# Optimization experiments

Hardware: AMD Instinct MI355X
Metric: run time of the kernel (lower is better)

The kernel has to match this reference:

```python
import jax, jax.numpy as jnp
import numpy as np

N = 256
FEAT = 1024           # box_head.fc7.out_features
HID_REL = 256         # RelationProposalNetwork hidden_dim
GCN_HID = 256         # gcn_hidden
HEADS = 4
NUM_PARTS = 20
OUT = NUM_PARTS + 1
TOPK = 3
IN_GCN = FEAT + 4


def setup_inputs() -> dict:
    key = jax.random.key(0)
    ks = jax.random.split(key, 16)
    features = jax.random.normal(ks[0], (N, FEAT), jnp.float32)
    # valid pixel-space boxes (x1, y1, x2, y2) inside an 800x800 image
    xy = jax.random.uniform(ks[1], (N, 2), jnp.float32, 0.0, 700.0)
    wh = jax.random.uniform(ks[2], (N, 2), jnp.float32, 8.0, 100.0)
    boxes = jnp.concatenate([xy, xy + wh], axis=1)
    s = 0.02
    W_fc1 = jax.random.normal(ks[3], (2 * FEAT + 4, HID_REL), jnp.float32) * s
    b_fc1 = jnp.zeros((HID_REL,), jnp.float32)
    W_fc2 = jax.random.normal(ks[4], (HID_REL, 1), jnp.float32) * s
    b_fc2 = jnp.zeros((1,), jnp.float32)
    W1 = jax.random.normal(ks[5], (IN_GCN, HEADS * GCN_HID), jnp.float32) * s
    a_src1 = jax.random.normal(ks[6], (HEADS, GCN_HID), jnp.float32) * s
    a_dst1 = jax.random.normal(ks[7], (HEADS, GCN_HID), jnp.float32) * s
    b1 = jnp.zeros((HEADS * GCN_HID,), jnp.float32)
    W2 = jax.random.normal(ks[8], (HEADS * GCN_HID, OUT), jnp.float32) * s
    a_src2 = jax.random.normal(ks[9], (1, OUT), jnp.float32) * s
    a_dst2 = jax.random.normal(ks[10], (1, OUT), jnp.float32) * s
    b2 = jnp.zeros((OUT,), jnp.float32)
    return {
        "features": features, "boxes": boxes,
        "W_fc1": W_fc1, "b_fc1": b_fc1, "W_fc2": W_fc2, "b_fc2": b_fc2,
        "W1": W1, "a_src1": a_src1, "a_dst1": a_dst1, "b1": b1,
        "W2": W2, "a_src2": a_src2, "a_dst2": a_dst2, "b2": b2,
        "img_h": 800, "img_w": 800,
    }


def _gat_layer(x, W, a_src, a_dst, bias, s, t, n, heads, ch):
    # PyG GATConv: message flows edge_index[0] (s) -> edge_index[1] (t),
    # softmax over incoming edges of each target node t.
    h = (x @ W).reshape(n, heads, ch)                       # [n, H, C]
    e = jax.nn.leaky_relu(
        jnp.einsum("ehc,hc->eh", h[s], a_src)
        + jnp.einsum("ehc,hc->eh", h[t], a_dst), 0.2)        # [E, H]
    m = jnp.full((n, heads), -1e30, e.dtype).at[t].max(e)    # segment max
    p = jnp.exp(e - m[t])
    denom = jax.ops.segment_sum(p, t, num_segments=n)
    alpha = p / denom[t]                                     # [E, H]
    out = jax.ops.segment_sum(alpha[:, :, None] * h[s], t, num_segments=n)
    return out.reshape(n, heads * ch) + bias


def _forward(features, boxes, W_fc1, b_fc1, W_fc2, b_fc2,
             W1, a_src1, a_dst1, b1, W2, a_src2, a_dst2, b2, img_h, img_w):
    n = features.shape[0]
    # --- RelationProposalNetwork: dense O(N^2) pairwise MLP ---
    f1 = jnp.broadcast_to(features[:, None, :], (n, n, FEAT))
    f2 = jnp.broadcast_to(features[None, :, :], (n, n, FEAT))
    geom = jnp.abs(boxes[:, None, :] - boxes[None, :, :])    # [n, n, 4]
    pair = jnp.concatenate([f1, f2, geom], axis=-1)          # [n, n, 2052]
    hid = jax.nn.relu(pair @ W_fc1 + b_fc1)                  # [n, n, 256]
    rel = (hid @ W_fc2 + b_fc2)[..., 0]                      # [n, n]
    # --- top-k graph construction (drop first = self, as in source) ---
    idx = jax.lax.top_k(rel, TOPK + 1)[1][:, 1:]             # [n, topk]
    s_e = jnp.repeat(jnp.arange(n), TOPK)                    # edge_index[0]
    t_e = idx.reshape(-1)                                    # edge_index[1]
    loops = jnp.arange(n)                                    # GATConv add_self_loops
    s_e = jnp.concatenate([s_e, loops])
    t_e = jnp.concatenate([t_e, loops])
    # --- normalized box geometry node features ---
    scale = jnp.array([img_w, img_h, img_w, img_h], jnp.float32)
    nb = boxes / scale
    geomn = jnp.stack([nb[:, 0], nb[:, 1], nb[:, 2] - nb[:, 0], nb[:, 3] - nb[:, 1]], axis=1)
    gcn_in = jnp.concatenate([features, geomn], axis=1)      # [n, 1028]
    # --- AttentionalGCN: GAT(heads=4) -> ReLU -> GAT(heads=1) ---
    h1 = jax.nn.relu(_gat_layer(gcn_in, W1, a_src1, a_dst1, b1, s_e, t_e, n, HEADS, GCN_HID))
    logits = _gat_layer(h1, W2, a_src2, a_dst2, b2, s_e, t_e, n, 1, OUT)
    return logits


def reference(features, boxes, W_fc1, b_fc1, W_fc2, b_fc2,
              W1, a_src1, a_dst1, b1, W2, a_src2, a_dst2, b2, img_h, img_w):
    logits = _forward(features, boxes, W_fc1, b_fc1, W_fc2, b_fc2,
                      W1, a_src1, a_dst1, b1, W2, a_src2, a_dst2, b2, img_h, img_w)
    labels = jnp.argmax(logits, axis=1)
    return logits, labels
```

## Files before the change

kernel.cpp:

```cpp
#include <hip/hip_runtime.h>
#include <math.h>

#define NN 256
#define FEAT 1024
#define HIDR 256
#define HEADS 4
#define GCNH 256
#define M1 1024
#define OUTC 21
#define MAXDEG (NN + 1)
#define KC 16
#define KCH (FEAT / KC)
#define RB 16
#define FCOLS 1536

__global__ __launch_bounds__(256) void k_big(
        const float* __restrict__ feat, const float* __restrict__ Wfc1,
        const float* __restrict__ W1, float* __restrict__ P) {
    __shared__ float fS[RB][KCH];
    int rg = blockIdx.x, cgy = blockIdx.y, kc = blockIdx.z;
    int tid = threadIdx.x;
    int r0 = rg * RB, k0 = kc * KCH;
    for (int x = tid; x < RB * KCH; x += 256) {
        int r = x >> 6, kk = x & (KCH - 1);
        fS[r][kk] = feat[(size_t)(r0 + r) * FEAT + k0 + kk];
    }
    __syncthreads();
    int gc = cgy * 512 + tid * 2;
    const float* pW;
    int ld;
    if (gc < 256)      { pW = Wfc1 + (size_t)k0 * HIDR + gc;                  ld = HIDR; }
    else if (gc < 512) { pW = Wfc1 + (size_t)(FEAT + k0) * HIDR + (gc - 256); ld = HIDR; }
    else               { pW = W1   + (size_t)k0 * M1 + (gc - 512);            ld = M1;   }
    float2 acc[RB];
#pragma unroll
    for (int r = 0; r < RB; r++) { acc[r].x = 0.f; acc[r].y = 0.f; }
    float2 w0 = *(const float2*)(pW);
    float2 w1 = *(const float2*)(pW + ld);
    float2 w2 = *(const float2*)(pW + 2 * ld);
    float2 w3 = *(const float2*)(pW + 3 * ld);
    for (int kk = 0; kk < KCH; kk += 4) {
        pW += 4 * ld;
        float2 n0 = *(const float2*)(pW);
        float2 n1 = *(const float2*)(pW + ld);
        float2 n2 = *(const float2*)(pW + 2 * ld);
        float2 n3 = *(const float2*)(pW + 3 * ld);
#pragma unroll
        for (int r = 0; r < RB; r++) {
            float4 f = *(const float4*)&fS[r][kk];
            acc[r].x = fmaf(f.x, w0.x, acc[r].x); acc[r].y = fmaf(f.x, w0.y, acc[r].y);
            acc[r].x = fmaf(f.y, w1.x, acc[r].x); acc[r].y = fmaf(f.y, w1.y, acc[r].y);
            acc[r].x = fmaf(f.z, w2.x, acc[r].x); acc[r].y = fmaf(f.z, w2.y, acc[r].y);
            acc[r].x = fmaf(f.w, w3.x, acc[r].x); acc[r].y = fmaf(f.w, w3.y, acc[r].y);
        }
        w0 = n0; w1 = n1; w2 = n2; w3 = n3;
    }
    float* Pp = P + ((size_t)kc * NN + r0) * FCOLS + gc;
#pragma unroll
    for (int r = 0; r < RB; r++)
        *(float2*)(Pp + (size_t)r * FCOLS) = acc[r];
}

__global__ __launch_bounds__(384) void k_redfix(
        const float* __restrict__ P, const float* __restrict__ bfc1,
        const float* __restrict__ boxes, const int* __restrict__ imh,
        const int* __restrict__ imw, const float* __restrict__ W1,
        const float* __restrict__ as1, const float* __restrict__ ad1,
        float* __restrict__ A, float* __restrict__ BT4,
        float* __restrict__ hpre, float* __restrict__ es1,
        float* __restrict__ ed1, float* __restrict__ geomn) {
    __shared__ float gS[4];
    int row = blockIdx.x, tid = threadIdx.x;
    int c4 = tid * 4;
    const float* p = P + (size_t)row * FCOLS + c4;
    const size_t str = (size_t)NN * FCOLS;
    float4 a0 = *(const float4*)(p);
    float4 a1 = *(const float4*)(p + str);
    float4 a2 = *(const float4*)(p + 2 * str);
    float4 a3 = *(const float4*)(p + 3 * str);
#pragma unroll
    for (int q = 4; q < KC; q += 4) {
        float4 t0 = *(const float4*)(p + (size_t)q * str);
        float4 t1 = *(const float4*)(p + (size_t)(q + 1) * str);
        float4 t2 = *(const float4*)(p + (size_t)(q + 2) * str);
        float4 t3 = *(const float4*)(p + (size_t)(q + 3) * str);
        a0.x += t0.x; a0.y += t0.y; a0.z += t0.z; a0.w += t0.w;
        a1.x += t1.x; a1.y += t1.y; a1.z += t1.z; a1.w += t1.w;
        a2.x += t2.x; a2.y += t2.y; a2.z += t2.z; a2.w += t2.w;
        a3.x += t3.x; a3.y += t3.y; a3.z += t3.z; a3.w += t3.w;
    }
    float4 s;
    s.x = (a0.x + a1.x) + (a2.x + a3.x);
    s.y = (a0.y + a1.y) + (a2.y + a3.y);
    s.z = (a0.z + a1.z) + (a2.z + a3.z);
    s.w = (a0.w + a1.w) + (a2.w + a3.w);
    if (tid == 0) {
        float w = (float)imw[0], h = (float)imh[0];
        float x1 = boxes[row * 4 + 0] / w, y1 = boxes[row * 4 + 1] / h;
        float x2 = boxes[row * 4 + 2] / w, y2 = boxes[row * 4 + 3] / h;
        gS[0] = x1; gS[1] = y1; gS[2] = x2 - x1; gS[3] = y2 - y1;
        geomn[row * 4 + 0] = x1;
        geomn[row * 4 + 1] = y1;
        geomn[row * 4 + 2] = x2 - x1;
        geomn[row * 4 + 3] = y2 - y1;
    }
    __syncthreads();
    if (c4 < 256) {
        float4 b = *(const float4*)(bfc1 + c4);
        s.x += b.x; s.y += b.y; s.z += b.z; s.w += b.w;
        *(float4*)(A + (size_t)row * HIDR + c4) = s;
    } else if (c4 < 512) {
        int kk = c4 - 256;
        *(float4*)(BT4 + (size_t)(kk >> 2) * (NN * 4) + row * 4) = s;
    } else {
        int ch = c4 - 512;
        float g0 = gS[0], g1 = gS[1], g2 = gS[2], g3 = gS[3];
        float4 wv;
        wv = *(const float4*)(W1 + (size_t)(FEAT + 0) * M1 + ch);
        s.x = fmaf(g0, wv.x, s.x); s.y = fmaf(g0, wv.y, s.y);
        s.z = fmaf(g0, wv.z, s.z); s.w = fmaf(g0, wv.w, s.w);
        wv = *(const float4*)(W1 + (size_t)(FEAT + 1) * M1 + ch);
        s.x = fmaf(g1, wv.x, s.x); s.y = fmaf(g1, wv.y, s.y);
        s.z = fmaf(g1, wv.z, s.z); s.w = fmaf(g1, wv.w, s.w);
        wv = *(const float4*)(W1 + (size_t)(FEAT + 2) * M1 + ch);
        s.x = fmaf(g2, wv.x, s.x); s.y = fmaf(g2, wv.y, s.y);
        s.z = fmaf(g2, wv.z, s.z); s.w = fmaf(g2, wv.w, s.w);
        wv = *(const float4*)(W1 + (size_t)(FEAT + 3) * M1 + ch);
        s.x = fmaf(g3, wv.x, s.x); s.y = fmaf(g3, wv.y, s.y);
        s.z = fmaf(g3, wv.z, s.z); s.w = fmaf(g3, wv.w, s.w);
        *(float4*)(hpre + (size_t)row * M1 + ch) = s;
        float4 a = *(const float4*)(as1 + ch);
        float4 b = *(const float4*)(ad1 + ch);
        float ps = s.x * a.x + s.y * a.y + s.z * a.z + s.w * a.w;
        float pd = s.x * b.x + s.y * b.y + s.z * b.z + s.w * b.w;
#pragma unroll
        for (int o = 32; o > 0; o >>= 1) {
            ps += __shfl_down(ps, o);
            pd += __shfl_down(pd, o);
        }
        if ((tid & 63) == 0) {
            int head = (tid - 128) >> 6;
            es1[row * 4 + head] = ps;
            ed1[row * 4 + head] = pd;
        }
    }
}

__global__ __launch_bounds__(512) void k_reltopk(
        const float* __restrict__ A, const float* __restrict__ BT4,
        const float* __restrict__ boxes, const float* __restrict__ Wfc1,
        const float* __restrict__ Wfc2, int* __restrict__ idxTop) {
    __shared__ float As[HIDR], w2s[HIDR], wg0[HIDR], wg1[HIDR], wg2[HIDR], wg3[HIDR];
    __shared__ float sval[512];
    __shared__ unsigned long long swk[8];
    __shared__ int win;
    int i = blockIdx.x, tid = threadIdx.x;
    int j = tid & 255, half = tid >> 8;
    if (tid < 256) {
        As[tid]  = A[i * HIDR + tid];
        w2s[tid] = Wfc2[tid];
        wg0[tid] = Wfc1[(size_t)(2 * FEAT + 0) * HIDR + tid];
    } else {
        int q = tid - 256;
        wg1[q] = Wfc1[(size_t)(2 * FEAT + 1) * HIDR + q];
        wg2[q] = Wfc1[(size_t)(2 * FEAT + 2) * HIDR + q];
        wg3[q] = Wfc1[(size_t)(2 * FEAT + 3) * HIDR + q];
    }
    float bi0 = boxes[i * 4 + 0], bi1 = boxes[i * 4 + 1];
    float bi2 = boxes[i * 4 + 2], bi3 = boxes[i * 4 + 3];
    float g0 = fabsf(bi0 - boxes[j * 4 + 0]);
    float g1 = fabsf(bi1 - boxes[j * 4 + 1]);
    float g2 = fabsf(bi2 - boxes[j * 4 + 2]);
    float g3 = fabsf(bi3 - boxes[j * 4 + 3]);
    __syncthreads();
    int k0 = half * 128;
    const float* pB = BT4 + (size_t)(k0 >> 2) * (NN * 4) + j * 4;
    float acc = 0.f;
    for (int kk = k0; kk < k0 + 128; kk += 4) {
        float4 a4 = *(const float4*)&As[kk];
        float4 w4 = *(const float4*)&w2s[kk];
        float4 q0 = *(const float4*)&wg0[kk];
        float4 q1 = *(const float4*)&wg1[kk];
        float4 q2 = *(const float4*)&wg2[kk];
        float4 q3 = *(const float4*)&wg3[kk];
        float4 b4 = *(const float4*)pB;
        pB += NN * 4;
        float v;
        v = a4.x + b4.x; v = fmaf(g0, q0.x, v); v = fmaf(g1, q1.x, v);
        v = fmaf(g2, q2.x, v); v = fmaf(g3, q3.x, v);
        acc = fmaf(fmaxf(v, 0.f), w4.x, acc);
        v = a4.y + b4.y; v = fmaf(g0, q0.y, v); v = fmaf(g1, q1.y, v);
        v = fmaf(g2, q2.y, v); v = fmaf(g3, q3.y, v);
        acc = fmaf(fmaxf(v, 0.f), w4.y, acc);
        v = a4.z + b4.z; v = fmaf(g0, q0.z, v); v = fmaf(g1, q1.z, v);
        v = fmaf(g2, q2.z, v); v = fmaf(g3, q3.z, v);
        acc = fmaf(fmaxf(v, 0.f), w4.z, acc);
        v = a4.w + b4.w; v = fmaf(g0, q0.w, v); v = fmaf(g1, q1.w, v);
        v = fmaf(g2, q2.w, v); v = fmaf(g3, q3.w, v);
        acc = fmaf(fmaxf(v, 0.f), w4.w, acc);
    }
    sval[tid] = acc;
    __syncthreads();
    if (tid < 256) sval[tid] = sval[tid] + sval[tid + 256];
    __syncthreads();
    for (int r = 0; r < 4; r++) {
        unsigned long long key = 0ULL;
        if (tid < 256) {
            unsigned u = __float_as_uint(sval[tid]);
            u = (u & 0x80000000u) ? ~u : (u | 0x80000000u);
            key = ((unsigned long long)u << 32) | (unsigned)(NN - 1 - tid);
        }
#pragma unroll
        for (int o = 32; o > 0; o >>= 1) {
            unsigned long long nk = __shfl_down(key, o);
            if (nk > key) key = nk;
        }
        if ((tid & 63) == 0) swk[tid >> 6] = key;
        __syncthreads();
        if (tid == 0) {
            unsigned long long m = swk[0];
#pragma unroll
            for (int q = 1; q < 8; q++) if (swk[q] > m) m = swk[q];
            int wj = NN - 1 - (int)(m & 0xFFFFFFFFu);
            win = wj;
            if (r > 0) idxTop[i * 3 + (r - 1)] = wj;
        }
        __syncthreads();
        if (tid == win) sval[tid] = -1e38f;
        __syncthreads();
    }
}

__global__ __launch_bounds__(256) void k_gat1h2(
        const float* __restrict__ idxTopF, const float* __restrict__ hpre,
        const float* __restrict__ es1, const float* __restrict__ ed1,
        const float* __restrict__ b1, const float* __restrict__ W2,
        const float* __restrict__ as2, const float* __restrict__ ad2,
        int* __restrict__ deg, int* __restrict__ inlist,
        float* __restrict__ h2, float* __restrict__ es2,
        float* __restrict__ ed2) {
    const int* idxTop = (const int*)idxTopF;
    __shared__ int pfx[NN];
    __shared__ int lst[MAXDEG];
    __shared__ int dgS;
    __shared__ float sc[MAXDEG * 4];
    __shared__ float mh[4], dh[4];
    __shared__ float sh[M1];
    __shared__ float part[12 * OUTC];
    __shared__ float h2row[OUTC];
    int t = blockIdx.x, tid = threadIdx.x;
    int f = (idxTop[tid * 3 + 0] == t) | (idxTop[tid * 3 + 1] == t)
          | (idxTop[tid * 3 + 2] == t);
    pfx[tid] = f;
    __syncthreads();
    for (int o = 1; o < NN; o <<= 1) {
        int add = (tid >= o) ? pfx[tid - o] : 0;
        __syncthreads();
        pfx[tid] += add;
        __syncthreads();
    }
    if (f) {
        lst[pfx[tid] - 1] = tid;
        inlist[t * MAXDEG + (pfx[tid] - 1)] = tid;
    }
    if (tid == NN - 1) {
        int d = pfx[NN - 1];
        lst[d] = t;
        inlist[t * MAXDEG + d] = t;
        dgS = d + 1;
        deg[t] = d + 1;
    }
    __syncthreads();
    int dg = dgS;
    for (int p = tid; p < dg * 4; p += 256) {
        int e = p >> 2, h = p & 3;
        int s = lst[e];
        float v = es1[s * 4 + h] + ed1[t * 4 + h];
        sc[p] = v >= 0.f ? v : 0.2f * v;
    }
    __syncthreads();
    if (tid < 4) {
        float m = -1e30f;
        for (int e = 0; e < dg; e++) m = fmaxf(m, sc[e * 4 + tid]);
        float s = 0.f;
        for (int e = 0; e < dg; e++) s += expf(sc[e * 4 + tid] - m);
        mh[tid] = m; dh[tid] = s;
    }
    __syncthreads();
    for (int p = tid; p < dg * 4; p += 256) {
        int h = p & 3;
        sc[p] = expf(sc[p] - mh[h]) / dh[h];
    }
    __syncthreads();
    float acc[4] = {0.f, 0.f, 0.f, 0.f};
    for (int e = 0; e < dg; e++) {
        int s = lst[e];
        const float* hs = hpre + (size_t)s * M1;
#pragma unroll
        for (int q = 0; q < 4; q++)
            acc[q] = fmaf(sc[e * 4 + q], hs[q * GCNH + tid], acc[q]);
    }
#pragma unroll
    for (int q = 0; q < 4; q++) {
        int c = q * GCNH + tid;
        sh[c] = fmaxf(acc[q] + b1[c], 0.f);
    }
    __syncthreads();
    if (tid < 252) {
        int o = tid % OUTC, p = tid / OUTC;
        float a2 = 0.f;
        for (int d = p; d < M1; d += 12)
            a2 = fmaf(sh[d], W2[d * OUTC + o], a2);
        part[p * OUTC + o] = a2;
    }
    __syncthreads();
    if (tid < OUTC) {
        float s = 0.f;
        for (int p = 0; p < 12; p++) s += part[p * OUTC + tid];
        h2[t * OUTC + tid] = s;
        h2row[tid] = s;
    }
    __syncthreads();
    if (tid == 0) {
        float s = 0.f, dd = 0.f;
        for (int k = 0; k < OUTC; k++) {
            s = fmaf(h2row[k], as2[k], s);
            dd = fmaf(h2row[k], ad2[k], dd);
        }
        es2[t] = s; ed2[t] = dd;
    }
}

__global__ __launch_bounds__(64) void k_gat2(
        const float* __restrict__ h2, const float* __restrict__ es2,
        const float* __restrict__ ed2, const int* __restrict__ deg,
        const int* __restrict__ inlist, const float* __restrict__ b2,
        float* __restrict__ out) {
    __shared__ float sc[MAXDEG];
    __shared__ float md[2];
    __shared__ float lv[OUTC];
    int t = blockIdx.x, tid = threadIdx.x;
    int dg = deg[t];
    float edt = ed2[t];
    for (int p = tid; p < dg; p += 64) {
        int s = inlist[t * MAXDEG + p];
        float v = es2[s] + edt;
        sc[p] = v >= 0.f ? v : 0.2f * v;
    }
    __syncthreads();
    if (tid == 0) {
        float m = -1e30f;
        for (int e = 0; e < dg; e++) m = fmaxf(m, sc[e]);
        float s = 0.f;
        for (int e = 0; e < dg; e++) s += expf(sc[e] - m);
        md[0] = m; md[1] = s;
    }
    __syncthreads();
    if (tid < OUTC) {
        float acc = 0.f;
        for (int e = 0; e < dg; e++) {
            int s = inlist[t * MAXDEG + e];
            float a = expf(sc[e] - md[0]) / md[1];
            acc = fmaf(a, h2[s * OUTC + tid], acc);
        }
        float v = acc + b2[tid];
        out[t * OUTC + tid] = v;
        lv[tid] = v;
    }
    __syncthreads();
    if (tid == 0) {
        int best = 0;
        float bv = lv[0];
        for (int o = 1; o < OUTC; o++)
            if (lv[o] > bv) { bv = lv[o]; best = o; }
        out[NN * OUTC + t] = (float)best;
    }
}

extern "C" void kernel_launch(void* const* d_in, const int* in_sizes, int n_in,
                              void* d_out, int out_size, void* d_ws,
                              size_t ws_size, hipStream_t stream) {
    const float* feat  = (const float*)d_in[0];
    const float* boxes = (const float*)d_in[1];
    const float* Wfc1  = (const float*)d_in[2];
    const float* bfc1  = (const float*)d_in[3];
    const float* Wfc2  = (const float*)d_in[4];
    const float* bfc2  = (const float*)d_in[5];   (void)bfc2;
    const float* W1    = (const float*)d_in[6];
    const float* as1   = (const float*)d_in[7];
    const float* ad1   = (const float*)d_in[8];
    const float* b1    = (const float*)d_in[9];
    const float* W2    = (const float*)d_in[10];
    const float* as2   = (const float*)d_in[11];
    const float* ad2   = (const float*)d_in[12];
    const float* b2    = (const float*)d_in[13];
    const int*   imh   = (const int*)d_in[14];
    const int*   imw   = (const int*)d_in[15];

    float* ws = (float*)d_ws;
    float* P     = ws;  ws += KC * NN * FCOLS;
    float* A     = ws;  ws += NN * HIDR;
    float* BT4   = ws;  ws += NN * HIDR;
    float* hpre  = ws;  ws += NN * M1;
    float* es1   = ws;  ws += NN * 4;
    float* ed1   = ws;  ws += NN * 4;
    float* h2    = ws;  ws += NN * OUTC;
    float* es2   = ws;  ws += NN;
    float* ed2   = ws;  ws += NN;
    float* geomn = ws;  ws += NN * 4;
    int* deg     = (int*)ws;
    int* inlist  = deg + NN;
    int* idxTop  = inlist + NN * MAXDEG;

    float* out = (float*)d_out;

    k_big<<<dim3(NN / RB, 3, KC), 256, 0, stream>>>(feat, Wfc1, W1, P);
    k_redfix<<<NN, 384, 0, stream>>>(P, bfc1, boxes, imh, imw, W1, as1, ad1,
                                     A, BT4, hpre, es1, ed1, geomn);
    k_reltopk<<<NN, 512, 0, stream>>>(A, BT4, boxes, Wfc1, Wfc2, idxTop);
    k_gat1h2<<<NN, 256, 0, stream>>>((const float*)idxTop, hpre, es1, ed1,
                                     b1, W2, as2, ad2, deg, inlist,
                                     h2, es2, ed2);
    k_gat2<<<NN, 64, 0, stream>>>(h2, es2, ed2, deg, inlist, b2, out);
}
```

Baseline: 164.8 us.

## Fuse four post-GEMM kernels into one persistent kernel with grid barriers

Merges the reduce/fixup, relation top-k, first GAT layer and second GAT layer kernels into one 256-block kernel that uses an atomic-counter grid barrier between stages. The barrier counter is reset inside the preceding GEMM kernel. Per-node in-edge lists stay in shared memory instead of going through global deg/inlist arrays, and the A vector is kept in LDS. This removes three kernel launch gaps and some global traffic. In exchange it relies on all 256 blocks being co-resident and adds spin-wait cost at each barrier.

Result: slower. 193.1 us (+17.2%).

```diff
diff --git a/kernel.cpp b/kernel.cpp
--- a/kernel.cpp
+++ b/kernel.cpp
@@ -16,7 +16,11 @@
 
 __global__ __launch_bounds__(256) void k_big(
         const float* __restrict__ feat, const float* __restrict__ Wfc1,
-        const float* __restrict__ W1, float* __restrict__ P) {
+        const float* __restrict__ W1, float* __restrict__ P,
+        unsigned* bar) {
+    if (blockIdx.x == 0 && blockIdx.y == 0 && blockIdx.z == 0 &&
+        threadIdx.x == 0)
+        *bar = 0u;
     __shared__ float fS[RB][KCH];
     int rg = blockIdx.x, cgy = blockIdx.y, kc = blockIdx.z;
     int tid = threadIdx.x;
@@ -61,103 +65,130 @@
         *(float2*)(Pp + (size_t)r * FCOLS) = acc[r];
 }
 
-__global__ __launch_bounds__(384) void k_redfix(
+__device__ __forceinline__ void gsync(unsigned* bar, unsigned expected) {
+    __syncthreads();
+    if (threadIdx.x == 0) {
+        __threadfence();
+        atomicAdd(bar, 1u);
+        while (atomicAdd(bar, 0u) < expected)
+            __builtin_amdgcn_s_sleep(2);
+        __threadfence();
+    }
+    __syncthreads();
+}
+
+__global__ __launch_bounds__(512, 4) void k_fused(
         const float* __restrict__ P, const float* __restrict__ bfc1,
         const float* __restrict__ boxes, const int* __restrict__ imh,
         const int* __restrict__ imw, const float* __restrict__ W1,
         const float* __restrict__ as1, const float* __restrict__ ad1,
-        float* __restrict__ A, float* __restrict__ BT4,
-        float* __restrict__ hpre, float* __restrict__ es1,
-        float* __restrict__ ed1, float* __restrict__ geomn) {
+        const float* __restrict__ Wfc1, const float* __restrict__ Wfc2,
+        const float* __restrict__ b1, const float* __restrict__ W2,
+        const float* __restrict__ as2, const float* __restrict__ ad2,
+        const float* __restrict__ b2,
+        float* __restrict__ BT4, float* __restrict__ hpre,
+        float* __restrict__ es1, float* __restrict__ ed1,
+        int* __restrict__ idxTop, float* __restrict__ h2,
+        float* __restrict__ es2, float* __restrict__ ed2,
+        unsigned* bar, float* __restrict__ out) {
     __shared__ float gS[4];
+    __shared__ float As[HIDR], w2s[HIDR];
+    __shared__ float wg0[HIDR], wg1[HIDR], wg2[HIDR], wg3[HIDR];
+    __shared__ float sval[512];
+    __shared__ unsigned long long swk[8];
+    __shared__ int win;
+    __shared__ int pfx[NN];
+    __shared__ int lst[MAXDEG];
+    __shared__ int dgS;
+    __shared__ float sc[MAXDEG * 4];
+    __shared__ float mh[4], dh[4];
+    __shared__ float sh[M1];
+    __shared__ float part[24 * OUTC];
+    __shared__ float h2row[OUTC];
+    __shared__ float scD[MAXDEG];
+    __shared__ float md[2];
+    __shared__ float lv[OUTC];
+
     int row = blockIdx.x, tid = threadIdx.x;
+
     int c4 = tid * 4;
-    const float* p = P + (size_t)row * FCOLS + c4;
-    const size_t str = (size_t)NN * FCOLS;
-    float4 a0 = *(const float4*)(p);
-    float4 a1 = *(const float4*)(p + str);
-    float4 a2 = *(const float4*)(p + 2 * str);
-    float4 a3 = *(const float4*)(p + 3 * str);
-#pragma unroll
-    for (int q = 4; q < KC; q += 4) {
-        float4 t0 = *(const float4*)(p + (size_t)q * str);
-        float4 t1 = *(const float4*)(p + (size_t)(q + 1) * str);
-        float4 t2 = *(const float4*)(p + (size_t)(q + 2) * str);
-        float4 t3 = *(const float4*)(p + (size_t)(q + 3) * str);
-        a0.x += t0.x; a0.y += t0.y; a0.z += t0.z; a0.w += t0.w;
-        a1.x += t1.x; a1.y += t1.y; a1.z += t1.z; a1.w += t1.w;
-        a2.x += t2.x; a2.y += t2.y; a2.z += t2.z; a2.w += t2.w;
-        a3.x += t3.x; a3.y += t3.y; a3.z += t3.z; a3.w += t3.w;
-    }
-    float4 s;
-    s.x = (a0.x + a1.x) + (a2.x + a3.x);
-    s.y = (a0.y + a1.y) + (a2.y + a3.y);
-    s.z = (a0.z + a1.z) + (a2.z + a3.z);
-    s.w = (a0.w + a1.w) + (a2.w + a3.w);
+    bool actA = (tid < 384);
+    float4 s4;
+    if (actA) {
+        const float* p = P + (size_t)row * FCOLS + c4;
+        const size_t str = (size_t)NN * FCOLS;
+        float4 a0 = *(const float4*)(p);
+        float4 a1 = *(const float4*)(p + str);
+        float4 a2 = *(const float4*)(p + 2 * str);
+        float4 a3 = *(const float4*)(p + 3 * str);
+#pragma unroll
+        for (int q = 4; q < KC; q += 4) {
+            float4 t0 = *(const float4*)(p + (size_t)q * str);
+            float4 t1 = *(const float4*)(p + (size_t)(q + 1) * str);
+            float4 t2 = *(const float4*)(p + (size_t)(q + 2) * str);
+            float4 t3 = *(const float4*)(p + (size_t)(q + 3) * str);
+            a0.x += t0.x; a0.y += t0.y; a0.z += t0.z; a0.w += t0.w;
+            a1.x += t1.x; a1.y += t1.y; a1.z += t1.z; a1.w += t1.w;
+            a2.x += t2.x; a2.y += t2.y; a2.z += t2.z; a2.w += t2.w;
+            a3.x += t3.x; a3.y += t3.y; a3.z += t3.z; a3.w += t3.w;
+        }
+        s4.x = (a0.x + a1.x) + (a2.x + a3.x);
+        s4.y = (a0.y + a1.y) + (a2.y + a3.y);
+        s4.z = (a0.z + a1.z) + (a2.z + a3.z);
+        s4.w = (a0.w + a1.w) + (a2.w + a3.w);
+    }
     if (tid == 0) {
         float w = (float)imw[0], h = (float)imh[0];
         float x1 = boxes[row * 4 + 0] / w, y1 = boxes[row * 4 + 1] / h;
         float x2 = boxes[row * 4 + 2] / w, y2 = boxes[row * 4 + 3] / h;
         gS[0] = x1; gS[1] = y1; gS[2] = x2 - x1; gS[3] = y2 - y1;
-        geomn[row * 4 + 0] = x1;
-        geomn[row * 4 + 1] = y1;
-        geomn[row * 4 + 2] = x2 - x1;
-        geomn[row * 4 + 3] = y2 - y1;
-    }
-    __syncthreads();
-    if (c4 < 256) {
-        float4 b = *(const float4*)(bfc1 + c4);
-        s.x += b.x; s.y += b.y; s.z += b.z; s.w += b.w;
-        *(float4*)(A + (size_t)row * HIDR + c4) = s;
-    } else if (c4 < 512) {
-        int kk = c4 - 256;
-        *(float4*)(BT4 + (size_t)(kk >> 2) * (NN * 4) + row * 4) = s;
-    } else {
-        int ch = c4 - 512;
-        float g0 = gS[0], g1 = gS[1], g2 = gS[2], g3 = gS[3];
-        float4 wv;
-        wv = *(const float4*)(W1 + (size_t)(FEAT + 0) * M1 + ch);
-        s.x = fmaf(g0, wv.x, s.x); s.y = fmaf(g0, wv.y, s.y);
-        s.z = fmaf(g0, wv.z, s.z); s.w = fmaf(g0, wv.w, s.w);
-        wv = *(const float4*)(W1 + (size_t)(FEAT + 1) * M1 + ch);
-        s.x = fmaf(g1, wv.x, s.x); s.y = fmaf(g1, wv.y, s.y);
-        s.z = fmaf(g1, wv.z, s.z); s.w = fmaf(g1, wv.w, s.w);
-        wv = *(const float4*)(W1 + (size_t)(FEAT + 2) * M1 + ch);
-        s.x = fmaf(g2, wv.x, s.x); s.y = fmaf(g2, wv.y, s.y);
-        s.z = fmaf(g2, wv.z, s.z); s.w = fmaf(g2, wv.w, s.w);
-        wv = *(const float4*)(W1 + (size_t)(FEAT + 3) * M1 + ch);
-        s.x = fmaf(g3, wv.x, s.x); s.y = fmaf(g3, wv.y, s.y);
-        s.z = fmaf(g3, wv.z, s.z); s.w = fmaf(g3, wv.w, s.w);
-        *(float4*)(hpre + (size_t)row * M1 + ch) = s;
-        float4 a = *(const float4*)(as1 + ch);
-        float4 b = *(const float4*)(ad1 + ch);
-        float ps = s.x * a.x + s.y * a.y + s.z * a.z + s.w * a.w;
-        float pd = s.x * b.x + s.y * b.y + s.z * b.z + s.w * b.w;
-#pragma unroll
-        for (int o = 32; o > 0; o >>= 1) {
-            ps += __shfl_down(ps, o);
-            pd += __shfl_down(pd, o);
-        }
-        if ((tid & 63) == 0) {
-            int head = (tid - 128) >> 6;
-            es1[row * 4 + head] = ps;
-            ed1[row * 4 + head] = pd;
-        }
-    }
-}
-
-__global__ __launch_bounds__(512) void k_reltopk(
-        const float* __restrict__ A, const float* __restrict__ BT4,
-        const float* __restrict__ boxes, const float* __restrict__ Wfc1,
-        const float* __restrict__ Wfc2, int* __restrict__ idxTop) {
-    __shared__ float As[HIDR], w2s[HIDR], wg0[HIDR], wg1[HIDR], wg2[HIDR], wg3[HIDR];
-    __shared__ float sval[512];
-    __shared__ unsigned long long swk[8];
-    __shared__ int win;
-    int i = blockIdx.x, tid = threadIdx.x;
-    int j = tid & 255, half = tid >> 8;
+    }
+    __syncthreads();
+    if (actA) {
+        if (c4 < 256) {
+            float4 b = *(const float4*)(bfc1 + c4);
+            s4.x += b.x; s4.y += b.y; s4.z += b.z; s4.w += b.w;
+            *(float4*)(&As[c4]) = s4;
+        } else if (c4 < 512) {
+            int kk = c4 - 256;
+            *(float4*)(BT4 + (size_t)(kk >> 2) * (NN * 4) + row * 4) = s4;
+        } else {
+            int ch = c4 - 512;
+            float g0 = gS[0], g1 = gS[1], g2 = gS[2], g3 = gS[3];
+            float4 wv;
+            wv = *(const float4*)(W1 + (size_t)(FEAT + 0) * M1 + ch);
+            s4.x = fmaf(g0, wv.x, s4.x); s4.y = fmaf(g0, wv.y, s4.y);
+            s4.z = fmaf(g0, wv.z, s4.z); s4.w = fmaf(g0, wv.w, s4.w);
+            wv = *(const float4*)(W1 + (size_t)(FEAT + 1) * M1 + ch);
+            s4.x = fmaf(g1, wv.x, s4.x); s4.y = fmaf(g1, wv.y, s4.y);
+            s4.z = fmaf(g1, wv.z, s4.z); s4.w = fmaf(g1, wv.w, s4.w);
+            wv = *(const float4*)(W1 + (size_t)(FEAT + 2) * M1 + ch);
+            s4.x = fmaf(g2, wv.x, s4.x); s4.y = fmaf(g2, wv.y, s4.y);
+            s4.z = fmaf(g2, wv.z, s4.z); s4.w = fmaf(g2, wv.w, s4.w);
+            wv = *(const float4*)(W1 + (size_t)(FEAT + 3) * M1 + ch);
+            s4.x = fmaf(g3, wv.x, s4.x); s4.y = fmaf(g3, wv.y, s4.y);
+            s4.z = fmaf(g3, wv.z, s4.z); s4.w = fmaf(g3, wv.w, s4.w);
+            *(float4*)(hpre + (size_t)row * M1 + ch) = s4;
+            float4 a = *(const float4*)(as1 + ch);
+            float4 b = *(const float4*)(ad1 + ch);
+            float ps = s4.x * a.x + s4.y * a.y + s4.z * a.z + s4.w * a.w;
+            float pd = s4.x * b.x + s4.y * b.y + s4.z * b.z + s4.w * b.w;
+#pragma unroll
+            for (int o = 32; o > 0; o >>= 1) {
+                ps += __shfl_down(ps, o);
+                pd += __shfl_down(pd, o);
+            }
+            if ((tid & 63) == 0) {
+                int head = (tid - 128) >> 6;
+                es1[row * 4 + head] = ps;
+                ed1[row * 4 + head] = pd;
+            }
+        }
+    }
+
+    gsync(bar, NN);
+
     if (tid < 256) {
-        As[tid]  = A[i * HIDR + tid];
         w2s[tid] = Wfc2[tid];
         wg0[tid] = Wfc1[(size_t)(2 * FEAT + 0) * HIDR + tid];
     } else {
@@ -166,40 +197,43 @@
         wg2[q] = Wfc1[(size_t)(2 * FEAT + 2) * HIDR + q];
         wg3[q] = Wfc1[(size_t)(2 * FEAT + 3) * HIDR + q];
     }
-    float bi0 = boxes[i * 4 + 0], bi1 = boxes[i * 4 + 1];
-    float bi2 = boxes[i * 4 + 2], bi3 = boxes[i * 4 + 3];
+    int j = tid & 255, half = tid >> 8;
+    float bi0 = boxes[row * 4 + 0], bi1 = boxes[row * 4 + 1];
+    float bi2 = boxes[row * 4 + 2], bi3 = boxes[row * 4 + 3];
     float g0 = fabsf(bi0 - boxes[j * 4 + 0]);
     float g1 = fabsf(bi1 - boxes[j * 4 + 1]);
     float g2 = fabsf(bi2 - boxes[j * 4 + 2]);
     float g3 = fabsf(bi3 - boxes[j * 4 + 3]);
     __syncthreads();
-    int k0 = half * 128;
-    const float* pB = BT4 + (size_t)(k0 >> 2) * (NN * 4) + j * 4;
-    float acc = 0.f;
-    for (int kk = k0; kk < k0 + 128; kk += 4) {
-        float4 a4 = *(const float4*)&As[kk];
-        float4 w4 = *(const float4*)&w2s[kk];
-        float4 q0 = *(const float4*)&wg0[kk];
-        float4 q1 = *(const float4*)&wg1[kk];
-        float4 q2 = *(const float4*)&wg2[kk];
-        float4 q3 = *(const float4*)&wg3[kk];
-        float4 b4 = *(const float4*)pB;
-        pB += NN * 4;
-        float v;
-        v = a4.x + b4.x; v = fmaf(g0, q0.x, v); v = fmaf(g1, q1.x, v);
-        v = fmaf(g2, q2.x, v); v = fmaf(g3, q3.x, v);
-        acc = fmaf(fmaxf(v, 0.f), w4.x, acc);
-        v = a4.y + b4.y; v = fmaf(g0, q0.y, v); v = fmaf(g1, q1.y, v);
-        v = fmaf(g2, q2.y, v); v = fmaf(g3, q3.y, v);
-        acc = fmaf(fmaxf(v, 0.f), w4.y, acc);
-        v = a4.z + b4.z; v = fmaf(g0, q0.z, v); v = fmaf(g1, q1.z, v);
-        v = fmaf(g2, q2.z, v); v = fmaf(g3, q3.z, v);
-        acc = fmaf(fmaxf(v, 0.f), w4.z, acc);
-        v = a4.w + b4.w; v = fmaf(g0, q0.w, v); v = fmaf(g1, q1.w, v);
-        v = fmaf(g2, q2.w, v); v = fmaf(g3, q3.w, v);
-        acc = fmaf(fmaxf(v, 0.f), w4.w, acc);
-    }
-    sval[tid] = acc;
+    {
+        int k0 = half * 128;
+        const float* pB = BT4 + (size_t)(k0 >> 2) * (NN * 4) + j * 4;
+        float acc = 0.f;
+        for (int kk = k0; kk < k0 + 128; kk += 4) {
+            float4 a4 = *(const float4*)&As[kk];
+            float4 w4 = *(const float4*)&w2s[kk];
+            float4 q0 = *(const float4*)&wg0[kk];
+            float4 q1 = *(const float4*)&wg1[kk];
+            float4 q2 = *(const float4*)&wg2[kk];
+            float4 q3 = *(const float4*)&wg3[kk];
+            float4 b4 = *(const float4*)pB;
+            pB += NN * 4;
+            float v;
+            v = a4.x + b4.x; v = fmaf(g0, q0.x, v); v = fmaf(g1, q1.x, v);
+            v = fmaf(g2, q2.x, v); v = fmaf(g3, q3.x, v);
+            acc = fmaf(fmaxf(v, 0.f), w4.x, acc);
+            v = a4.y + b4.y; v = fmaf(g0, q0.y, v); v = fmaf(g1, q1.y, v);
+            v = fmaf(g2, q2.y, v); v = fmaf(g3, q3.y, v);
+            acc = fmaf(fmaxf(v, 0.f), w4.y, acc);
+            v = a4.z + b4.z; v = fmaf(g0, q0.z, v); v = fmaf(g1, q1.z, v);
+            v = fmaf(g2, q2.z, v); v = fmaf(g3, q3.z, v);
+            acc = fmaf(fmaxf(v, 0.f), w4.z, acc);
+            v = a4.w + b4.w; v = fmaf(g0, q0.w, v); v = fmaf(g1, q1.w, v);
+            v = fmaf(g2, q2.w, v); v = fmaf(g3, q3.w, v);
+            acc = fmaf(fmaxf(v, 0.f), w4.w, acc);
+        }
+        sval[tid] = acc;
+    }
     __syncthreads();
     if (tid < 256) sval[tid] = sval[tid] + sval[tid + 256];
     __syncthreads();
@@ -223,148 +257,122 @@
             for (int q = 1; q < 8; q++) if (swk[q] > m) m = swk[q];
             int wj = NN - 1 - (int)(m & 0xFFFFFFFFu);
             win = wj;
-            if (r > 0) idxTop[i * 3 + (r - 1)] = wj;
+            if (r > 0) idxTop[row * 3 + (r - 1)] = wj;
         }
         __syncthreads();
         if (tid == win) sval[tid] = -1e38f;
         __syncthreads();
     }
-}
-
-__global__ __launch_bounds__(256) void k_gat1h2(
-        const float* __restrict__ idxTopF, const float* __restrict__ hpre,
-        const float* __restrict__ es1, const float* __restrict__ ed1,
-        const float* __restrict__ b1, const float* __restrict__ W2,
-        const float* __restrict__ as2, const float* __restrict__ ad2,
-        int* __restrict__ deg, int* __restrict__ inlist,
-        float* __restrict__ h2, float* __restrict__ es2,
-        float* __restrict__ ed2) {
-    const int* idxTop = (const int*)idxTopF;
-    __shared__ int pfx[NN];
-    __shared__ int lst[MAXDEG];
-    __shared__ int dgS;
-    __shared__ float sc[MAXDEG * 4];
-    __shared__ float mh[4], dh[4];
-    __shared__ float sh[M1];
-    __shared__ float part[12 * OUTC];
-    __shared__ float h2row[OUTC];
-    int t = blockIdx.x, tid = threadIdx.x;
-    int f = (idxTop[tid * 3 + 0] == t) | (idxTop[tid * 3 + 1] == t)
-          | (idxTop[tid * 3 + 2] == t);
-    pfx[tid] = f;
+
+    gsync(bar, 2 * NN);
+
+    int f = 0;
+    if (tid < 256) {
+        f = (idxTop[tid * 3 + 0] == row) | (idxTop[tid * 3 + 1] == row)
+          | (idxTop[tid * 3 + 2] == row);
+        pfx[tid] = f;
+    }
     __syncthreads();
     for (int o = 1; o < NN; o <<= 1) {
-        int add = (tid >= o) ? pfx[tid - o] : 0;
+        int add = 0;
+        if (tid < 256 && tid >= o) add = pfx[tid - o];
         __syncthreads();
-        pfx[tid] += add;
+        if (tid < 256) pfx[tid] += add;
         __syncthreads();
     }
-    if (f) {
-        lst[pfx[tid] - 1] = tid;
-        inlist[t * MAXDEG + (pfx[tid] - 1)] = tid;
-    }
+    if (tid < 256 && f) lst[pfx[tid] - 1] = tid;
     if (tid == NN - 1) {
         int d = pfx[NN - 1];
-        lst[d] = t;
-        inlist[t * MAXDEG + d] = t;
+        lst[d] = row;
         dgS = d + 1;
-        deg[t] = d + 1;
     }
     __syncthreads();
     int dg = dgS;
-    for (int p = tid; p < dg * 4; p += 256) {
-        int e = p >> 2, h = p & 3;
+    for (int p = tid; p < dg * 4; p += 512) {
+        int e = p >> 2, hq = p & 3;
         int s = lst[e];
-        float v = es1[s * 4 + h] + ed1[t * 4 + h];
+        float v = es1[s * 4 + hq] + ed1[row * 4 + hq];
         sc[p] = v >= 0.f ? v : 0.2f * v;
     }
     __syncthreads();
     if (tid < 4) {
         float m = -1e30f;
         for (int e = 0; e < dg; e++) m = fmaxf(m, sc[e * 4 + tid]);
-        float s = 0.f;
-        for (int e = 0; e < dg; e++) s += expf(sc[e * 4 + tid] - m);
-        mh[tid] = m; dh[tid] = s;
-    }
-    __syncthreads();
-    for (int p = tid; p < dg * 4; p += 256) {
-        int h = p & 3;
-        sc[p] = expf(sc[p] - mh[h]) / dh[h];
-    }
-    __syncthreads();
-    float acc[4] = {0.f, 0.f, 0.f, 0.f};
-    for (int e = 0; e < dg; e++) {
-        int s = lst[e];
-        const float* hs = hpre + (size_t)s * M1;
-#pragma unroll
-        for (int q = 0; q < 4; q++)
-            acc[q] = fmaf(sc[e * 4 + q], hs[q * GCNH + tid], acc[q]);
-    }
-#pragma unroll
-    for (int q = 0; q < 4; q++) {
-        int c = q * GCNH + tid;
-        sh[c] = fmaxf(acc[q] + b1[c], 0.f);
-    }
-    __syncthreads();
-    if (tid < 252) {
-        int o = tid % OUTC, p = tid / OUTC;
+        float ssum = 0.f;
+        for (int e = 0; e < dg; e++) ssum += expf(sc[e * 4 + tid] - m);
+        mh[tid] = m; dh[tid] = ssum;
+    }
+    __syncthreads();
+    for (int p = tid; p < dg * 4; p += 512) {
+        int hq = p & 3;
+        sc[p] = expf(sc[p] - mh[hq]) / dh[hq];
+    }
+    __syncthreads();
+    {
+        int col = tid & 255, hh = (tid >> 8) * 2;
+        float acc0 = 0.f, acc1 = 0.f;
+        for (int e = 0; e < dg; e++) {
+            int s = lst[e];
+            const float* hs = hpre + (size_t)s * M1;
+            acc0 = fmaf(sc[e * 4 + hh],     hs[hh * GCNH + col],       acc0);
+            acc1 = fmaf(sc[e * 4 + hh + 1], hs[(hh + 1) * GCNH + col], acc1);
+        }
+        int c0 = hh * GCNH + col, c1 = (hh + 1) * GCNH + col;
+        sh[c0] = fmaxf(acc0 + b1[c0], 0.f);
+        sh[c1] = fmaxf(acc1 + b1[c1], 0.f);
+    }
+    __syncthreads();
+    if (tid < 504) {
+        int o = tid % OUTC, pq = tid / OUTC;
         float a2 = 0.f;
-        for (int d = p; d < M1; d += 12)
+        for (int d = pq; d < M1; d += 24)
             a2 = fmaf(sh[d], W2[d * OUTC + o], a2);
-        part[p * OUTC + o] = a2;
+        part[pq * OUTC + o] = a2;
     }
     __syncthreads();
     if (tid < OUTC) {
-        float s = 0.f;
-        for (int p = 0; p < 12; p++) s += part[p * OUTC + tid];
-        h2[t * OUTC + tid] = s;
-        h2row[tid] = s;
+        float ssum = 0.f;
+        for (int pq = 0; pq < 24; pq++) ssum += part[pq * OUTC + tid];
+        h2[row * OUTC + tid] = ssum;
+        h2row[tid] = ssum;
     }
     __syncthreads();
     if (tid == 0) {
-        float s = 0.f, dd = 0.f;
+        float ssum = 0.f, dd = 0.f;
         for (int k = 0; k < OUTC; k++) {
-            s = fmaf(h2row[k], as2[k], s);
+            ssum = fmaf(h2row[k], as2[k], ssum);
             dd = fmaf(h2row[k], ad2[k], dd);
         }
-        es2[t] = s; ed2[t] = dd;
-    }
-}
-
-__global__ __launch_bounds__(64) void k_gat2(
-        const float* __restrict__ h2, const float* __restrict__ es2,
-        const float* __restrict__ ed2, const int* __restrict__ deg,
-        const int* __restrict__ inlist, const float* __restrict__ b2,
-        float* __restrict__ out) {
-    __shared__ float sc[MAXDEG];
-    __shared__ float md[2];
-    __shared__ float lv[OUTC];
-    int t = blockIdx.x, tid = threadIdx.x;
-    int dg = deg[t];
-    float edt = ed2[t];
-    for (int p = tid; p < dg; p += 64) {
-        int s = inlist[t * MAXDEG + p];
+        es2[row] = ssum; ed2[row] = dd;
+    }
+
+    gsync(bar, 3 * NN);
+
+    int dgT = dgS;
+    float edt = ed2[row];
+    for (int p = tid; p < dgT; p += 512) {
+        int s = lst[p];
         float v = es2[s] + edt;
-        sc[p] = v >= 0.f ? v : 0.2f * v;
+        scD[p] = v >= 0.f ? v : 0.2f * v;
     }
     __syncthreads();
     if (tid == 0) {
         float m = -1e30f;
-        for (int e = 0; e < dg; e++) m = fmaxf(m, sc[e]);
-        float s = 0.f;
-        for (int e = 0; e < dg; e++) s += expf(sc[e] - m);
-        md[0] = m; md[1] = s;
+        for (int e = 0; e < dgT; e++) m = fmaxf(m, scD[e]);
+        float ssum = 0.f;
+        for (int e = 0; e < dgT; e++) ssum += expf(scD[e] - m);
+        md[0] = m; md[1] = ssum;
     }
     __syncthreads();
     if (tid < OUTC) {
         float acc = 0.f;
-        for (int e = 0; e < dg; e++) {
-            int s = inlist[t * MAXDEG + e];
-            float a = expf(sc[e] - md[0]) / md[1];
+        for (int e = 0; e < dgT; e++) {
+            int s = lst[e];
+            float a = expf(scD[e] - md[0]) / md[1];
             acc = fmaf(a, h2[s * OUTC + tid], acc);
         }
         float v = acc + b2[tid];
-        out[t * OUTC + tid] = v;
+        out[row * OUTC + tid] = v;
         lv[tid] = v;
     }
     __syncthreads();
@@ -373,7 +381,7 @@
         float bv = lv[0];
         for (int o = 1; o < OUTC; o++)
             if (lv[o] > bv) { bv = lv[o]; best = o; }
-        out[NN * OUTC + t] = (float)best;
+        out[NN * OUTC + row] = (float)best;
     }
 }
 
@@ -399,7 +407,6 @@
 
     float* ws = (float*)d_ws;
     float* P     = ws;  ws += KC * NN * FCOLS;
-    float* A     = ws;  ws += NN * HIDR;
     float* BT4   = ws;  ws += NN * HIDR;
     float* hpre  = ws;  ws += NN * M1;
     float* es1   = ws;  ws += NN * 4;
@@ -407,19 +414,14 @@
     float* h2    = ws;  ws += NN * OUTC;
     float* es2   = ws;  ws += NN;
     float* ed2   = ws;  ws += NN;
-    float* geomn = ws;  ws += NN * 4;
-    int* deg     = (int*)ws;
-    int* inlist  = deg + NN;
-    int* idxTop  = inlist + NN * MAXDEG;
+    int* idxTop  = (int*)ws;  ws += NN * 3;
+    unsigned* bar = (unsigned*)ws;
 
     float* out = (float*)d_out;
 
-    k_big<<<dim3(NN / RB, 3, KC), 256, 0, stream>>>(feat, Wfc1, W1, P);
-    k_redfix<<<NN, 384, 0, stream>>>(P, bfc1, boxes, imh, imw, W1, as1, ad1,
-                                     A, BT4, hpre, es1, ed1, geomn);
-    k_reltopk<<<NN, 512, 0, stream>>>(A, BT4, boxes, Wfc1, Wfc2, idxTop);
-    k_gat1h2<<<NN, 256, 0, stream>>>((const float*)idxTop, hpre, es1, ed1,
-                                     b1, W2, as2, ad2, deg, inlist,
-                                     h2, es2, ed2);
-    k_gat2<<<NN, 64, 0, stream>>>(h2, es2, ed2, deg, inlist, b2, out);
+    k_big<<<dim3(NN / RB, 3, KC), 256, 0, stream>>>(feat, Wfc1, W1, P, bar);
+    k_fused<<<NN, 512, 0, stream>>>(P, bfc1, boxes, imh, imw, W1, as1, ad1,
+                                    Wfc1, Wfc2, b1, W2, as2, ad2, b2,
+                                    BT4, hpre, es1, ed1, idxTop, h2, es2, ed2,
+                                    bar, out);
 }
```
